# Kernel optimization log

Measured on AMD Instinct MI355X. Metric: run time of the kernel, lower is better.

## Reference

```python
import jax, jax.numpy as jnp
import numpy as np


def setup_inputs() -> dict:
    key = jax.random.key(0)
    ks = jax.random.split(key, 7)
    B, D, K, L = 32768, 256, 8, 4
    s = 1.0 / np.sqrt(D)
    return {
        "x": jax.random.normal(ks[0], (B, D), jnp.float32),
        "gate_W": jax.random.normal(ks[1], (D, K), jnp.float32) * s,
        "gate_b": jax.random.normal(ks[2], (K,), jnp.float32) * s,
        "block_W": jax.random.normal(ks[3], (L, K, D, D), jnp.float32) * s,
        "block_b": jax.random.normal(ks[4], (L, K, D), jnp.float32) * s,
        "out_W": jax.random.normal(ks[5], (K, D, D), jnp.float32) * s,
        "out_b": jax.random.normal(ks[6], (K, D), jnp.float32) * s,
    }


def _moie_block(x, alpha, W, b):
    # x: (B, in), alpha: (B, K), W: (K, in, out), b: (K, out)
    z = jnp.einsum('bi,kio->bko', x, W) + b[None]        # (B, K, out)
    return jnp.einsum('bk,bko->bo', alpha, z)            # alpha-weighted sum over experts


def reference(x, gate_W, gate_b, block_W, block_b, out_W, out_b):
    # standard gating: softmax(Linear(x)); same alpha reused at every layer
    alpha = jax.nn.softmax(x @ gate_W + gate_b, axis=-1)  # (B, K)
    h = x
    num_layers = block_W.shape[0]
    for i in range(num_layers):
        h = jax.nn.relu(_moie_block(h, alpha, block_W[i], block_b[i]))
    # output block, no activation
    return _moie_block(h, alpha, out_W, out_b)
```

## Files before the change

kernel.cpp:

```cpp
#include <hip/hip_runtime.h>
#include <hip/hip_bf16.h>

typedef __attribute__((ext_vector_type(8))) _Float16 h8v;
typedef __attribute__((ext_vector_type(4))) float f4v;

__device__ __forceinline__ ushort f16bits(float f) {
    _Float16 h = (_Float16)f;
    return __builtin_bit_cast(unsigned short, h);
}

#define GL2LDS16(g, l) __builtin_amdgcn_global_load_lds( \
    (const __attribute__((address_space(1))) void*)(g),  \
    (__attribute__((address_space(3))) void*)(l), 16, 0, 0)

__global__ __launch_bounds__(256) void gate_kernel(
    const float* __restrict__ x, const float* __restrict__ gW,
    const float* __restrict__ gb, float* __restrict__ alpha)
{
    int lane = threadIdx.x & 63;
    int wave = threadIdx.x >> 6;
    int row = blockIdx.x * 4 + wave;
    float4 xv = *(const float4*)(x + (size_t)row * 256 + lane * 4);
    const float* xp = (const float*)&xv;
    float p[8];
#pragma unroll
    for (int k = 0; k < 8; ++k) p[k] = 0.f;
#pragma unroll
    for (int j = 0; j < 4; ++j) {
        float xs = xp[j];
        const float* wr = gW + (lane * 4 + j) * 8;
#pragma unroll
        for (int k = 0; k < 8; ++k) p[k] = fmaf(xs, wr[k], p[k]);
    }
#pragma unroll
    for (int off = 32; off > 0; off >>= 1) {
#pragma unroll
        for (int k = 0; k < 8; ++k) p[k] += __shfl_xor(p[k], off);
    }
    float m = -1e30f;
#pragma unroll
    for (int k = 0; k < 8; ++k) { p[k] += gb[k]; m = fmaxf(m, p[k]); }
    float s = 0.f;
#pragma unroll
    for (int k = 0; k < 8; ++k) { p[k] = expf(p[k] - m); s += p[k]; }
    if (lane < 8) alpha[(size_t)row * 8 + lane] = p[lane] / s;
}

__global__ __launch_bounds__(256) void prep_weights(
    const float* __restrict__ blockW, const float* __restrict__ outW,
    ushort* __restrict__ Wh)
{
    int mat = blockIdx.x >> 4;
    int tile = blockIdx.x & 15;
    int i0 = (tile >> 2) * 64, o0 = (tile & 3) * 64;
    const float* src = (mat < 32) ? (blockW + (size_t)mat * 65536)
                                  : (outW + (size_t)(mat - 32) * 65536);
    __shared__ float tl[64][65];
    int r = threadIdx.x >> 2, c0 = (threadIdx.x & 3) * 16;
#pragma unroll
    for (int e = 0; e < 16; e += 4) {
        float4 v = *(const float4*)(src + (size_t)(i0 + r) * 256 + o0 + c0 + e);
        tl[r][c0 + e + 0] = v.x; tl[r][c0 + e + 1] = v.y;
        tl[r][c0 + e + 2] = v.z; tl[r][c0 + e + 3] = v.w;
    }
    __syncthreads();
    int oc = threadIdx.x >> 2, ic0 = (threadIdx.x & 3) * 16;
    uint hp[8];
#pragma unroll
    for (int e = 0; e < 16; e += 2) {
        ushort h0 = f16bits(tl[ic0 + e][oc]);
        ushort h1 = f16bits(tl[ic0 + e + 1][oc]);
        hp[e >> 1] = (uint)h0 | ((uint)h1 << 16);
    }
    size_t base = ((size_t)(mat * 256 + o0 + oc)) * 256 + i0 + ic0;
    *(uint4*)(Wh + base)     = make_uint4(hp[0], hp[1], hp[2], hp[3]);
    *(uint4*)(Wh + base + 8) = make_uint4(hp[4], hp[5], hp[6], hp[7]);
}

template<bool RELU>
__global__ __launch_bounds__(256, 2) void moie_gemm(
    const float* __restrict__ Hin, float* __restrict__ Hout,
    const ushort* __restrict__ Wh,
    const float* __restrict__ bias, const float* __restrict__ alpha)
{
    __shared__ __align__(16) ushort Ah[64 * 256];
    __shared__ __align__(16) ushort Bh[2][256 * 32];

    const int tid  = threadIdx.x;
    const int lane = tid & 63;
    const int wid  = tid >> 6;
    const int m0   = blockIdx.x * 64;
    const int wcol0 = wid * 64;
    const int kgl = lane >> 4;
    const int fr  = lane & 15;

    float areg[4][8];
#pragma unroll
    for (int im = 0; im < 4; ++im) {
        const float4* ap = (const float4*)(alpha + (size_t)(m0 + im * 16 + fr) * 8);
        float4 a0 = ap[0], a1 = ap[1];
        areg[im][0] = a0.x; areg[im][1] = a0.y; areg[im][2] = a0.z; areg[im][3] = a0.w;
        areg[im][4] = a1.x; areg[im][5] = a1.y; areg[im][6] = a1.z; areg[im][7] = a1.w;
    }

    int bgoff[4];
#pragma unroll
    for (int q = 0; q < 4; ++q) {
        int c = q * 256 + tid;
        int n = c >> 2;
        int kg = (c & 3) ^ ((n >> 1) & 3);
        bgoff[q] = n * 256 + kg * 8;
    }
    int boff[4];
#pragma unroll
    for (int in = 0; in < 4; ++in) {
        int n = wcol0 + in * 16 + fr;
        boff[in] = n * 32 + (kgl ^ ((n >> 1) & 3)) * 8;
    }

#pragma unroll
    for (int q = 0; q < 4; ++q)
        GL2LDS16(Wh + bgoff[q], &Bh[0][(q * 256 + wid * 64) * 8]);

    {
        const int r0  = tid >> 6;
        const int kk  = (tid & 63) * 4;
        const int kg  = kk >> 3;
        const int klo = kk & 7;
#pragma unroll
        for (int p = 0; p < 16; ++p) {
            int row = p * 4 + r0;
            float4 v = *(const float4*)(Hin + (size_t)(m0 + row) * 256 + kk);
            uint2 pk;
            pk.x = (uint)f16bits(v.x) | ((uint)f16bits(v.y) << 16);
            pk.y = (uint)f16bits(v.z) | ((uint)f16bits(v.w) << 16);
            *(uint2*)&Ah[row * 256 + (kg ^ (row & 7)) * 8 + klo] = pk;
        }
    }

    f4v acc[4][4];
#pragma unroll
    for (int a = 0; a < 4; ++a)
#pragma unroll
        for (int b = 0; b < 4; ++b) acc[a][b] = (f4v){0.f, 0.f, 0.f, 0.f};

    h8v afc[4];

#pragma unroll 1
    for (int t = 0; t < 64; ++t) {
        const int cur = t & 1;
        __syncthreads();
        if (t < 63) {
            const int tn  = t + 1;
            const int en  = tn & 7;
            const int ki0 = (tn >> 3) * 32;
#pragma unroll
            for (int q = 0; q < 4; ++q)
                GL2LDS16(Wh + (size_t)en * 65536 + bgoff[q] + ki0,
                         &Bh[cur ^ 1][(q * 256 + wid * 64) * 8]);
        }
        if ((t & 7) == 0) {
            const int kg0 = (t >> 3) * 4;
#pragma unroll
            for (int im = 0; im < 4; ++im) {
                int row = im * 16 + fr;
                afc[im] = *(const h8v*)&Ah[row * 256 + ((kg0 + kgl) ^ (row & 7)) * 8];
            }
        }
        const int e = t & 7;
        h8v as[4];
#pragma unroll
        for (int im = 0; im < 4; ++im) {
            _Float16 ah = (_Float16)areg[im][e];
            as[im] = afc[im] * ah;
        }
        h8v bf[4];
#pragma unroll
        for (int in = 0; in < 4; ++in)
            bf[in] = *(const h8v*)&Bh[cur][boff[in]];
#pragma unroll
        for (int im = 0; im < 4; ++im)
#pragma unroll
            for (int in = 0; in < 4; ++in)
                acc[im][in] = __builtin_amdgcn_mfma_f32_16x16x32_f16(as[im], bf[in], acc[im][in], 0, 0, 0);
    }

    float bv[4][8];
#pragma unroll
    for (int in = 0; in < 4; ++in) {
        int col = wcol0 + in * 16 + fr;
#pragma unroll
        for (int k = 0; k < 8; ++k) bv[in][k] = bias[k * 256 + col];
    }
#pragma unroll
    for (int im = 0; im < 4; ++im) {
#pragma unroll
        for (int j = 0; j < 4; ++j) {
            int row = m0 + im * 16 + kgl * 4 + j;
            const float4* ap = (const float4*)(alpha + (size_t)row * 8);
            float4 a0 = ap[0], a1 = ap[1];
            float a8[8] = {a0.x, a0.y, a0.z, a0.w, a1.x, a1.y, a1.z, a1.w};
#pragma unroll
            for (int in = 0; in < 4; ++in) {
                int col = wcol0 + in * 16 + fr;
                float be = 0.f;
#pragma unroll
                for (int k = 0; k < 8; ++k) be = fmaf(a8[k], bv[in][k], be);
                float v = acc[im][in][j] + be;
                if (RELU) v = fmaxf(v, 0.f);
                Hout[(size_t)row * 256 + col] = v;
            }
        }
    }
}

extern "C" void kernel_launch(void* const* d_in, const int* in_sizes, int n_in,
                              void* d_out, int out_size, void* d_ws, size_t ws_size,
                              hipStream_t stream)
{
    const float* x      = (const float*)d_in[0];
    const float* gW     = (const float*)d_in[1];
    const float* gb     = (const float*)d_in[2];
    const float* blockW = (const float*)d_in[3];
    const float* blockB = (const float*)d_in[4];
    const float* outW   = (const float*)d_in[5];
    const float* outB   = (const float*)d_in[6];
    float* out = (float*)d_out;

    char* ws = (char*)d_ws;
    float*  alpha = (float*)ws;
    ushort* Wh    = (ushort*)(ws + (1 << 20));

    prep_weights<<<640, 256, 0, stream>>>(blockW, outW, Wh);
    gate_kernel<<<8192, 256, 0, stream>>>(x, gW, gb, alpha);

    const size_t WL = (size_t)8 * 65536;
    moie_gemm<true ><<<512, 256, 0, stream>>>(x,   out, Wh,          blockB,            alpha);
    moie_gemm<true ><<<512, 256, 0, stream>>>(out, out, Wh + 1 * WL, blockB + 1 * 2048, alpha);
    moie_gemm<true ><<<512, 256, 0, stream>>>(out, out, Wh + 2 * WL, blockB + 2 * 2048, alpha);
    moie_gemm<true ><<<512, 256, 0, stream>>>(out, out, Wh + 3 * WL, blockB + 3 * 2048, alpha);
    moie_gemm<false><<<512, 256, 0, stream>>>(out, out, Wh + 4 * WL, outB,              alpha);
}
```

Baseline: 290.7 us.

## Load expert weights straight into registers in MFMA fragment layout

The weight prep kernel now writes each expert's fp16 weights in a per-(expert, k-chunk) layout that matches the MFMA B-fragment order. The GEMM then reads B fragments directly from global memory (L2) into a double-buffered register set, which removes the LDS staging buffer and the per-step __syncthreads. It also restructures the loop as k-chunk outer, expert inner, and raises wave priority around the MFMA bursts. The cost is that every wave issues its own global loads, which puts more traffic on L2. There is also less latency hiding than with async LDS staging, because loads are only one step ahead.

Measured after the change: 357.6 us. +23.0%, slower.

```diff
diff --git a/kernel.cpp b/kernel.cpp
--- a/kernel.cpp
+++ b/kernel.cpp
@@ -8,10 +8,6 @@
     _Float16 h = (_Float16)f;
     return __builtin_bit_cast(unsigned short, h);
 }
-
-#define GL2LDS16(g, l) __builtin_amdgcn_global_load_lds( \
-    (const __attribute__((address_space(1))) void*)(g),  \
-    (__attribute__((address_space(3))) void*)(l), 16, 0, 0)
 
 __global__ __launch_bounds__(256) void gate_kernel(
     const float* __restrict__ x, const float* __restrict__ gW,
@@ -48,43 +44,35 @@
 
 __global__ __launch_bounds__(256) void prep_weights(
     const float* __restrict__ blockW, const float* __restrict__ outW,
-    ushort* __restrict__ Wh)
-{
-    int mat = blockIdx.x >> 4;
-    int tile = blockIdx.x & 15;
-    int i0 = (tile >> 2) * 64, o0 = (tile & 3) * 64;
-    const float* src = (mat < 32) ? (blockW + (size_t)mat * 65536)
-                                  : (outW + (size_t)(mat - 32) * 65536);
-    __shared__ float tl[64][65];
-    int r = threadIdx.x >> 2, c0 = (threadIdx.x & 3) * 16;
-#pragma unroll
-    for (int e = 0; e < 16; e += 4) {
-        float4 v = *(const float4*)(src + (size_t)(i0 + r) * 256 + o0 + c0 + e);
-        tl[r][c0 + e + 0] = v.x; tl[r][c0 + e + 1] = v.y;
-        tl[r][c0 + e + 2] = v.z; tl[r][c0 + e + 3] = v.w;
-    }
-    __syncthreads();
-    int oc = threadIdx.x >> 2, ic0 = (threadIdx.x & 3) * 16;
-    uint hp[8];
-#pragma unroll
-    for (int e = 0; e < 16; e += 2) {
-        ushort h0 = f16bits(tl[ic0 + e][oc]);
-        ushort h1 = f16bits(tl[ic0 + e + 1][oc]);
-        hp[e >> 1] = (uint)h0 | ((uint)h1 << 16);
-    }
-    size_t base = ((size_t)(mat * 256 + o0 + oc)) * 256 + i0 + ic0;
-    *(uint4*)(Wh + base)     = make_uint4(hp[0], hp[1], hp[2], hp[3]);
-    *(uint4*)(Wh + base + 8) = make_uint4(hp[4], hp[5], hp[6], hp[7]);
+    ushort* __restrict__ Wg)
+{
+    const int m = blockIdx.x >> 3;
+    const int g = blockIdx.x & 7;
+    const float* src = (m < 32) ? (blockW + (size_t)m * 65536)
+                                : (outW + (size_t)(m - 32) * 65536);
+    const int o = threadIdx.x;
+    uint pk[16];
+#pragma unroll
+    for (int kp = 0; kp < 16; ++kp) {
+        float f0 = src[(size_t)(g * 32 + 2 * kp) * 256 + o];
+        float f1 = src[(size_t)(g * 32 + 2 * kp + 1) * 256 + o];
+        pk[kp] = (uint)f16bits(f0) | ((uint)f16bits(f1) << 16);
+    }
+    size_t base = (size_t)(m >> 3) * 524288 + (size_t)((m & 7) * 8 + g) * 8192
+                + (size_t)o * 32;
+    *(uint4*)(Wg + base)      = make_uint4(pk[0],  pk[1],  pk[2],  pk[3]);
+    *(uint4*)(Wg + base + 8)  = make_uint4(pk[4],  pk[5],  pk[6],  pk[7]);
+    *(uint4*)(Wg + base + 16) = make_uint4(pk[8],  pk[9],  pk[10], pk[11]);
+    *(uint4*)(Wg + base + 24) = make_uint4(pk[12], pk[13], pk[14], pk[15]);
 }
 
 template<bool RELU>
 __global__ __launch_bounds__(256, 2) void moie_gemm(
     const float* __restrict__ Hin, float* __restrict__ Hout,
-    const ushort* __restrict__ Wh,
+    const ushort* __restrict__ Wg,
     const float* __restrict__ bias, const float* __restrict__ alpha)
 {
     __shared__ __align__(16) ushort Ah[64 * 256];
-    __shared__ __align__(16) ushort Bh[2][256 * 32];
 
     const int tid  = threadIdx.x;
     const int lane = tid & 63;
@@ -103,25 +91,6 @@
         areg[im][4] = a1.x; areg[im][5] = a1.y; areg[im][6] = a1.z; areg[im][7] = a1.w;
     }
 
-    int bgoff[4];
-#pragma unroll
-    for (int q = 0; q < 4; ++q) {
-        int c = q * 256 + tid;
-        int n = c >> 2;
-        int kg = (c & 3) ^ ((n >> 1) & 3);
-        bgoff[q] = n * 256 + kg * 8;
-    }
-    int boff[4];
-#pragma unroll
-    for (int in = 0; in < 4; ++in) {
-        int n = wcol0 + in * 16 + fr;
-        boff[in] = n * 32 + (kgl ^ ((n >> 1) & 3)) * 8;
-    }
-
-#pragma unroll
-    for (int q = 0; q < 4; ++q)
-        GL2LDS16(Wh + bgoff[q], &Bh[0][(q * 256 + wid * 64) * 8]);
-
     {
         const int r0  = tid >> 6;
         const int kk  = (tid & 63) * 4;
@@ -131,12 +100,15 @@
         for (int p = 0; p < 16; ++p) {
             int row = p * 4 + r0;
             float4 v = *(const float4*)(Hin + (size_t)(m0 + row) * 256 + kk);
-            uint2 pk;
-            pk.x = (uint)f16bits(v.x) | ((uint)f16bits(v.y) << 16);
-            pk.y = (uint)f16bits(v.z) | ((uint)f16bits(v.w) << 16);
-            *(uint2*)&Ah[row * 256 + (kg ^ (row & 7)) * 8 + klo] = pk;
-        }
-    }
+            uint2 pkv;
+            pkv.x = (uint)f16bits(v.x) | ((uint)f16bits(v.y) << 16);
+            pkv.y = (uint)f16bits(v.z) | ((uint)f16bits(v.w) << 16);
+            *(uint2*)&Ah[row * 256 + (kg ^ (row & 7)) * 8 + klo] = pkv;
+        }
+    }
+    __syncthreads();
+
+    const ushort* Wslice = Wg + (size_t)wcol0 * 32 + (size_t)(fr * 4 + kgl) * 8;
 
     f4v acc[4][4];
 #pragma unroll
@@ -144,45 +116,49 @@
 #pragma unroll
         for (int b = 0; b < 4; ++b) acc[a][b] = (f4v){0.f, 0.f, 0.f, 0.f};
 
+    h8v bfs[2][4];
+#pragma unroll
+    for (int in = 0; in < 4; ++in) {
+        bfs[0][in] = *(const h8v*)(Wslice + (size_t)0 * 8192 + in * 512);
+        bfs[1][in] = *(const h8v*)(Wslice + (size_t)8 * 8192 + in * 512);
+    }
+
     h8v afc[4];
 
 #pragma unroll 1
-    for (int t = 0; t < 64; ++t) {
-        const int cur = t & 1;
-        __syncthreads();
-        if (t < 63) {
-            const int tn  = t + 1;
-            const int en  = tn & 7;
-            const int ki0 = (tn >> 3) * 32;
-#pragma unroll
-            for (int q = 0; q < 4; ++q)
-                GL2LDS16(Wh + (size_t)en * 65536 + bgoff[q] + ki0,
-                         &Bh[cur ^ 1][(q * 256 + wid * 64) * 8]);
-        }
-        if ((t & 7) == 0) {
-            const int kg0 = (t >> 3) * 4;
+    for (int ki = 0; ki < 8; ++ki) {
+        const int kg0 = ki * 4;
+#pragma unroll
+        for (int im = 0; im < 4; ++im) {
+            int row = im * 16 + fr;
+            afc[im] = *(const h8v*)&Ah[row * 256 + ((kg0 + kgl) ^ (row & 7)) * 8];
+        }
+#pragma unroll
+        for (int e = 0; e < 8; ++e) {
+            const int set = e & 1;
+            h8v as[4];
 #pragma unroll
             for (int im = 0; im < 4; ++im) {
-                int row = im * 16 + fr;
-                afc[im] = *(const h8v*)&Ah[row * 256 + ((kg0 + kgl) ^ (row & 7)) * 8];
+                _Float16 ah = (_Float16)areg[im][e];
+                as[im] = afc[im] * ah;
             }
-        }
-        const int e = t & 7;
-        h8v as[4];
-#pragma unroll
-        for (int im = 0; im < 4; ++im) {
-            _Float16 ah = (_Float16)areg[im][e];
-            as[im] = afc[im] * ah;
-        }
-        h8v bf[4];
-#pragma unroll
-        for (int in = 0; in < 4; ++in)
-            bf[in] = *(const h8v*)&Bh[cur][boff[in]];
-#pragma unroll
-        for (int im = 0; im < 4; ++im)
+            __builtin_amdgcn_s_setprio(1);
+#pragma unroll
+            for (int im = 0; im < 4; ++im)
+#pragma unroll
+                for (int in = 0; in < 4; ++in)
+                    acc[im][in] = __builtin_amdgcn_mfma_f32_16x16x32_f16(
+                        as[im], bfs[set][in], acc[im][in], 0, 0, 0);
+            __builtin_amdgcn_s_setprio(0);
+            int ne, nki;
+            if (e < 6) { ne = e + 2; nki = ki; }
+            else       { ne = e - 6; nki = ki + 1; }
+            if (nki > 7) { nki = 7; ne = 7; }
+            const ushort* tp = Wslice + (size_t)(ne * 8 + nki) * 8192;
 #pragma unroll
             for (int in = 0; in < 4; ++in)
-                acc[im][in] = __builtin_amdgcn_mfma_f32_16x16x32_f16(as[im], bf[in], acc[im][in], 0, 0, 0);
+                bfs[set][in] = *(const h8v*)(tp + in * 512);
+        }
     }
 
     float bv[4][8];
@@ -229,15 +205,15 @@
 
     char* ws = (char*)d_ws;
     float*  alpha = (float*)ws;
-    ushort* Wh    = (ushort*)(ws + (1 << 20));
-
-    prep_weights<<<640, 256, 0, stream>>>(blockW, outW, Wh);
+    ushort* Wg    = (ushort*)(ws + (1 << 20));
+
+    prep_weights<<<320, 256, 0, stream>>>(blockW, outW, Wg);
     gate_kernel<<<8192, 256, 0, stream>>>(x, gW, gb, alpha);
 
-    const size_t WL = (size_t)8 * 65536;
-    moie_gemm<true ><<<512, 256, 0, stream>>>(x,   out, Wh,          blockB,            alpha);
-    moie_gemm<true ><<<512, 256, 0, stream>>>(out, out, Wh + 1 * WL, blockB + 1 * 2048, alpha);
-    moie_gemm<true ><<<512, 256, 0, stream>>>(out, out, Wh + 2 * WL, blockB + 2 * 2048, alpha);
-    moie_gemm<true ><<<512, 256, 0, stream>>>(out, out, Wh + 3 * WL, blockB + 3 * 2048, alpha);
-    moie_gemm<false><<<512, 256, 0, stream>>>(out, out, Wh + 4 * WL, outB,              alpha);
-}
+    const size_t WL = (size_t)524288;
+    moie_gemm<true ><<<512, 256, 0, stream>>>(x,   out, Wg,          blockB,            alpha);
+    moie_gemm<true ><<<512, 256, 0, stream>>>(out, out, Wg + 1 * WL, blockB + 1 * 2048, alpha);
+    moie_gemm<true ><<<512, 256, 0, stream>>>(out, out, Wg + 2 * WL, blockB + 2 * 2048, alpha);
+    moie_gemm<true ><<<512, 256, 0, stream>>>(out, out, Wg + 3 * WL, blockB + 3 * 2048, alpha);
+    moie_gemm<false><<<512, 256, 0, stream>>>(out, out, Wg + 4 * WL, outB,              alpha);
+}
```
